# Optimization experiments

Hardware: AMD Instinct MI355X
Metric: run time of the kernel (lower is better)

The kernel has to match this reference:

```python
import jax, jax.numpy as jnp
import numpy as np

B, N, D, H = 4, 2048, 512, 8
DH = D // H
EPS = 1e-6


def setup_inputs() -> dict:
    key = jax.random.key(0)
    ks = jax.random.split(key, 12)
    s = 1.0 / np.sqrt(D)
    return {
        "x": jax.random.normal(ks[0], (B, N, D), jnp.float32),
        "attn_bias": jax.random.normal(ks[1], (B, 1, N, N), jnp.float32),
        "Wq": jax.random.normal(ks[2], (D, D), jnp.float32) * s,
        "bq": jnp.zeros((D,), jnp.float32),
        "Wk": jax.random.normal(ks[3], (D, D), jnp.float32) * s,
        "bk": jnp.zeros((D,), jnp.float32),
        "Wv": jax.random.normal(ks[4], (D, D), jnp.float32) * s,
        "bv": jnp.zeros((D,), jnp.float32),
        "Wo": jax.random.normal(ks[5], (D, D), jnp.float32) * s,
        "bo": jnp.zeros((D,), jnp.float32),
        "q_gamma": jnp.ones((DH,), jnp.float32),
        "q_beta": jnp.zeros((DH,), jnp.float32),
        "k_gamma": jnp.ones((DH,), jnp.float32),
        "k_beta": jnp.zeros((DH,), jnp.float32),
    }


def _layernorm(x, gamma, beta):
    mu = jnp.mean(x, axis=-1, keepdims=True)
    var = jnp.var(x, axis=-1, keepdims=True)
    return (x - mu) * jax.lax.rsqrt(var + EPS) * gamma + beta


def reference(x, attn_bias, Wq, bq, Wk, bk, Wv, bv, Wo, bo,
              q_gamma, q_beta, k_gamma, k_beta):
    b, n, d = x.shape
    # project and split heads: (B, H, N, DH)
    def heads(W, bias):
        return (x @ W.T + bias).reshape(b, n, H, DH).transpose(0, 2, 1, 3)
    q = heads(Wq, bq)
    k = heads(Wk, bk)
    v = heads(Wv, bv)
    q = _layernorm(q, q_gamma, q_beta)
    k = _layernorm(k, k_gamma, k_beta)
    scores = jnp.einsum('bhqd,bhkd->bhqk', q, k) / np.sqrt(DH)
    scores = scores + attn_bias  # (B,1,N,N) broadcasts over heads
    attn = jax.nn.softmax(scores, axis=-1)
    out = jnp.einsum('bhqk,bhkd->bhqd', attn, v)
    out = out.transpose(0, 2, 1, 3).reshape(b, n, d)
    return out @ Wo.T + bo
```

## Files before the change

kernel.cpp:

```cpp
#include <hip/hip_runtime.h>

typedef __attribute__((ext_vector_type(8))) short short8;
typedef __attribute__((ext_vector_type(4))) float f32x4;
typedef __attribute__((ext_vector_type(4))) int i32x4;
typedef __attribute__((ext_vector_type(4))) unsigned short u16x4;
typedef __attribute__((ext_vector_type(8))) unsigned short u16x8;
typedef __attribute__((ext_vector_type(2))) unsigned int u32x2;

#define B_  4
#define N_  2048
#define D_  512
#define H_  8
#define DH_ 64
#define M_  (B_ * N_)

__device__ __forceinline__ unsigned short f2bf(float f) {
    union { float f; unsigned u; } un; un.f = f;
    unsigned r = un.u + 0x7FFFu + ((un.u >> 16) & 1u);
    return (unsigned short)(r >> 16);
}
__device__ __forceinline__ float exp2fast(float x) {
#if __has_builtin(__builtin_amdgcn_exp2f)
    return __builtin_amdgcn_exp2f(x);
#else
    float r; asm("v_exp_f32 %0, %1" : "=v"(r) : "v"(x)); return r;
#endif
}
__device__ __forceinline__ unsigned cvtpk_bf16(float lo, float hi) {
    unsigned r;
    asm("v_cvt_pk_bf16_f32 %0, %1, %2" : "=v"(r) : "v"(lo), "v"(hi));
    return r;
}
__device__ __forceinline__ float max3f(float a, float b, float c) {
    return fmaxf(fmaxf(a, b), c);
}

typedef __attribute__((address_space(1))) const void gvoid;
typedef __attribute__((address_space(3))) void svoid;
__device__ __forceinline__ void load16_lds(const void* g, void* s) {
    __builtin_amdgcn_global_load_lds((gvoid*)g, (svoid*)s, 16, 0, 0);
}

__global__ __launch_bounds__(256) void cvt_all(
    const float* __restrict__ x,
    const float* __restrict__ W0, const float* __restrict__ W1,
    const float* __restrict__ W2, const float* __restrict__ W3,
    unsigned short* __restrict__ xb, unsigned short* __restrict__ Wb) {
    const int bx = blockIdx.x;
    const float* src;
    unsigned short* dst;
    int i;
    if (bx < 4096) {
        src = x; dst = xb;
        i = (bx * 256 + (int)threadIdx.x) * 4;
    } else {
        const int r = bx - 4096;
        const int sel = r >> 8;
        src = (sel == 0) ? W0 : (sel == 1) ? W1 : (sel == 2) ? W2 : W3;
        dst = Wb + (size_t)sel * D_ * D_;
        i = ((r & 255) * 256 + (int)threadIdx.x) * 4;
    }
    f32x4 v = *(const f32x4*)(src + i);
    u16x4 o;
    o[0] = f2bf(v[0]); o[1] = f2bf(v[1]); o[2] = f2bf(v[2]); o[3] = f2bf(v[3]);
    *(u16x4*)(dst + i) = o;
}

template <bool F32OUT, bool LNF>
__global__ __launch_bounds__(256, 2) void gemm_nt(
    const unsigned short* __restrict__ A,
    const unsigned short* __restrict__ W,
    const float* __restrict__ Bv0,
    const float* __restrict__ Bv1,
    const float* __restrict__ Bv2,
    const float* __restrict__ g0, const float* __restrict__ be0,
    const float* __restrict__ g1, const float* __restrict__ be1,
    unsigned short* __restrict__ outb,
    float* __restrict__ outf)
{
    const int mt = blockIdx.x;
    const int nt = blockIdx.y;
    const int sel = nt >> 2;
    const unsigned short* Wp = W + (size_t)sel * D_ * D_;
    const float* Bv = (sel == 0) ? Bv0 : (sel == 1) ? Bv1 : Bv2;
    const int n0 = (nt & 3) * 128;

    __shared__ __align__(16) unsigned short As[128 * 32];
    __shared__ __align__(16) unsigned short Bs[128 * 32];

    const int tid = threadIdx.x;
    const int w   = tid >> 6;
    const int l   = tid & 63;
    const int l15 = l & 15;
    const int qd  = l >> 4;
    const int wr  = w >> 1;
    const int wc  = w & 1;

    int srow[2], scol[2];
#pragma unroll
    for (int c = 0; c < 2; ++c) {
        const int g   = (w * 2 + c) * 64 + l;
        const int row = g >> 2;
        srow[c] = row;
        scol[c] = ((g & 3) ^ (row & 3)) * 8;
    }

    f32x4 acc[4][4];
#pragma unroll
    for (int i = 0; i < 4; ++i)
#pragma unroll
        for (int j = 0; j < 4; ++j)
            acc[i][j] = (f32x4){0.f, 0.f, 0.f, 0.f};

    const int swz = qd ^ (l15 & 3);

    for (int k0 = 0; k0 < D_; k0 += 32) {
        __syncthreads();
#pragma unroll
        for (int c = 0; c < 2; ++c) {
            load16_lds(A  + (size_t)(mt * 128 + srow[c]) * D_ + k0 + scol[c],
                       As + (w * 2 + c) * 512);
            load16_lds(Wp + (size_t)(n0 + srow[c]) * D_ + k0 + scol[c],
                       Bs + (w * 2 + c) * 512);
        }
        __syncthreads();

        short8 af[4], bfr[4];
#pragma unroll
        for (int rt = 0; rt < 4; ++rt)
            af[rt] = *(const short8*)&As[(wr * 64 + rt * 16 + l15) * 32 + swz * 8];
#pragma unroll
        for (int ct = 0; ct < 4; ++ct)
            bfr[ct] = *(const short8*)&Bs[(wc * 64 + ct * 16 + l15) * 32 + swz * 8];
#pragma unroll
        for (int rt = 0; rt < 4; ++rt)
#pragma unroll
            for (int ct = 0; ct < 4; ++ct)
                acc[rt][ct] = __builtin_amdgcn_mfma_f32_16x16x32_bf16(
                    af[rt], bfr[ct], acc[rt][ct], 0, 0, 0);
    }

    const float* gam = (sel == 0) ? g0 : g1;
    const float* bet = (sel == 0) ? be0 : be1;
    float gv[4], bv2[4];
    if (LNF) {
#pragma unroll
        for (int ct = 0; ct < 4; ++ct) { gv[ct] = gam[ct * 16 + l15]; bv2[ct] = bet[ct * 16 + l15]; }
    }

#pragma unroll
    for (int rt = 0; rt < 4; ++rt) {
        float v[4][4];
#pragma unroll
        for (int ct = 0; ct < 4; ++ct) {
            const float bias = Bv[n0 + wc * 64 + ct * 16 + l15];
#pragma unroll
            for (int r = 0; r < 4; ++r) v[ct][r] = acc[rt][ct][r] + bias;
        }
        if (LNF && sel < 2) {
#pragma unroll
            for (int r = 0; r < 4; ++r) {
                float s  = v[0][r] + v[1][r] + v[2][r] + v[3][r];
                float s2 = v[0][r]*v[0][r] + v[1][r]*v[1][r] + v[2][r]*v[2][r] + v[3][r]*v[3][r];
#pragma unroll
                for (int o = 1; o <= 8; o <<= 1) {
                    s  += __shfl_xor(s, o);
                    s2 += __shfl_xor(s2, o);
                }
                const float mu  = s * 0.015625f;
                const float var = s2 * 0.015625f - mu * mu;
                const float rs  = rsqrtf(var + 1e-6f);
#pragma unroll
                for (int ct = 0; ct < 4; ++ct)
                    v[ct][r] = (v[ct][r] - mu) * rs * gv[ct] + bv2[ct];
            }
        }
#pragma unroll
        for (int ct = 0; ct < 4; ++ct) {
            const int col  = n0 + wc * 64 + ct * 16 + l15;
            const int row0 = mt * 128 + wr * 64 + rt * 16 + qd * 4;
#pragma unroll
            for (int r = 0; r < 4; ++r) {
                const size_t oidx = (size_t)(row0 + r) * D_ + col;
                if (F32OUT) outf[oidx] = v[ct][r];
                else        outb[(size_t)sel * M_ * D_ + oidx] = f2bf(v[ct][r]);
            }
        }
    }
}

__global__ __launch_bounds__(256) void pack_kv(
    const unsigned short* __restrict__ K, const unsigned short* __restrict__ V,
    unsigned short* __restrict__ Kt, unsigned short* __restrict__ Vt2)
{
    const int nt = blockIdx.x, b = blockIdx.y;
    const int tid = threadIdx.x;
    __shared__ __align__(16) unsigned short Vl[64][520];

#pragma unroll
    for (int i = 0; i < 16; ++i) {
        const int c = i * 256 + tid;
        const int row = c >> 6, ch = c & 63;
        const size_t srow = ((size_t)(b * N_ + nt * 64 + row)) * D_ + ch * 8;
        i32x4 kd = *(const i32x4*)(K + srow);
        const int h = ch >> 3, dc = ch & 7;
        *(i32x4*)(Kt + ((((size_t)(b * 8 + h) * 32 + nt) * 64 + row) * 64) + dc * 8) = kd;
        i32x4 vd = *(const i32x4*)(V + srow);
        *(i32x4*)&Vl[row][ch * 8] = vd;
    }
    __syncthreads();
#pragma unroll
    for (int i = 0; i < 16; ++i) {
        const int c = i * 256 + tid;
        const int h = c >> 9, r = c & 511;
        const int dh = r >> 3, kc = r & 7;
        u16x4 o0, o1;
#pragma unroll
        for (int j = 0; j < 4; ++j) o0[j] = Vl[kc * 8 + j][h * 64 + dh];
#pragma unroll
        for (int j = 0; j < 4; ++j) o1[j] = Vl[kc * 8 + 4 + j][h * 64 + dh];
        const int t = kc >> 1;
        const int col0 = (t & 2) * 16 + (kc & 1) * 16 + (t & 1) * 4;
        const size_t rowbase = ((((size_t)(b * 8 + h) * 32 + nt) * 64 + dh) * 64);
        *(u16x4*)(Vt2 + rowbase + col0)     = o0;
        *(u16x4*)(Vt2 + rowbase + col0 + 8) = o1;
    }
}

__global__ __launch_bounds__(512, 4) void attn12(
    const unsigned short* __restrict__ Qm,
    const unsigned short* __restrict__ Kt,
    const unsigned short* __restrict__ Vt2,
    const float* __restrict__ Bias,
    unsigned short* __restrict__ AO)
{
    const int qt = blockIdx.x;
    const int h  = blockIdx.y;
    const int b  = blockIdx.z;
    const int w  = threadIdx.x >> 6;
    const int l  = threadIdx.x & 63;
    const int l15 = l & 15;
    const int qd  = l >> 4;
    const int q0 = qt * 128 + w * 16;
    const float L2E = 1.4426950408889634f;

    __shared__ __align__(16) unsigned char smem[32768];

    const int c    = w * 64 + l;
    const int srow = c >> 3;
    const int sg   = (c & 7) ^ (srow & 7);
    const int soff = srow * 64 + sg * 8;
    const int sc16 = c * 16;

    short8 qf[2];
#pragma unroll
    for (int hf = 0; hf < 2; ++hf)
        qf[hf] = *(const short8*)(Qm +
            (size_t)(b * N_ + q0 + l15) * D_ + h * DH_ + hf * 32 + qd * 8);

    f32x4 Ot[4];
#pragma unroll
    for (int rt = 0; rt < 4; ++rt) Ot[rt] = (f32x4){0.f, 0.f, 0.f, 0.f};
    float m_i = -3.0e38f;
    f32x4 li4 = (f32x4){0.f, 0.f, 0.f, 0.f};

    const unsigned short* Ktile0 = Kt  + (((size_t)(b * 8 + h) * 32) * 64) * 64;
    const unsigned short* Vtile0 = Vt2 + (((size_t)(b * 8 + h) * 32) * 64) * 64;
    const float* biasQ = Bias + ((size_t)b * N_ + q0 + l15) * N_;

    load16_lds(Ktile0 + soff, smem + sc16);
    load16_lds(Vtile0 + soff, smem + 8192 + sc16);
    f32x4 brA[4], brB[4];
#pragma unroll
    for (int rt = 0; rt < 4; ++rt)
        brA[rt] = *(const f32x4*)(biasQ + rt * 16 + qd * 4);
    asm volatile("s_waitcnt vmcnt(0)" ::: "memory");

#define ATTN_ITER(KT, CUR, BRC, BRN) do {                                      \
    unsigned char* Kbc = smem + (CUR) * 16384;                                 \
    unsigned char* Vbc = Kbc + 8192;                                           \
    asm volatile("s_waitcnt vmcnt(4)" ::: "memory");                           \
    __builtin_amdgcn_s_barrier();                                              \
    __builtin_amdgcn_sched_barrier(0);                                         \
    if ((KT) < 31) {                                                           \
        const unsigned short* Kn = Ktile0 + (size_t)((KT) + 1) * 4096;         \
        const unsigned short* Vn = Vtile0 + (size_t)((KT) + 1) * 4096;         \
        unsigned char* KbN = smem + (((CUR) ^ 1)) * 16384;                     \
        load16_lds(Kn + soff, KbN + sc16);                                     \
        load16_lds(Vn + soff, KbN + 8192 + sc16);                              \
    }                                                                          \
    asm volatile("" ::: "memory");       \
    {                                                                          \
        const float* Bn = biasQ + (size_t)(((KT) < 31) ? (KT) + 1 : 31) * 64;  \
        _Pragma("unroll")                                                      \
        for (int rt = 0; rt < 4; ++rt)                                         \
            BRN[rt] = *(const f32x4*)(Bn + rt * 16 + qd * 4);                  \
    }                                                                          \
    short8 kf[4][2];                                                           \
    _Pragma("unroll")                                                          \
    for (int rt = 0; rt < 4; ++rt) {                                           \
        const int kv = rt * 16 + l15;                                          \
        _Pragma("unroll")                                                      \
        for (int hf = 0; hf < 2; ++hf) {                                       \
            const int cidx = (hf * 4 + qd) ^ (kv & 7);                         \
            kf[rt][hf] = *(const short8*)(Kbc + kv * 128 + cidx * 16);         \
        }                                                                      \
    }                                                                          \
    f32x4 St[4];                                                               \
    __builtin_amdgcn_s_setprio(1);                                             \
    _Pragma("unroll")                                                          \
    for (int rt = 0; rt < 4; ++rt) {                                           \
        f32x4 v = (f32x4){0.f, 0.f, 0.f, 0.f};                                 \
        v = __builtin_amdgcn_mfma_f32_16x16x32_bf16(kf[rt][0], qf[0], v, 0, 0, 0); \
        v = __builtin_amdgcn_mfma_f32_16x16x32_bf16(kf[rt][1], qf[1], v, 0, 0, 0); \
        St[rt] = v;                                                            \
    }                                                                          \
    __builtin_amdgcn_s_setprio(0);                                             \
    short8 vf[4][2];                                                           \
    _Pragma("unroll")                                                          \
    for (int rt = 0; rt < 4; ++rt) {                                           \
        const int dh = rt * 16 + l15;                                          \
        _Pragma("unroll")                                                      \
        for (int hf = 0; hf < 2; ++hf) {                                       \
            const int cidx = (hf * 4 + qd) ^ (dh & 7);                         \
            vf[rt][hf] = *(const short8*)(Vbc + dh * 128 + cidx * 16);         \
        }                                                                      \
    }                                                                          \
    unsigned wq[4][2];                                                         \
    {                                                                          \
        f32x4 sv[4];                                                           \
        _Pragma("unroll")                                                      \
        for (int rt = 0; rt < 4; ++rt)                                         \
            sv[rt] = St[rt] * 0.125f + BRC[rt];                                \
        float mx0 = max3f(sv[0][0], sv[0][1], sv[0][2]);                       \
        float mx1 = max3f(sv[0][3], sv[1][0], sv[1][1]);                       \
        float mx2 = max3f(sv[1][2], sv[1][3], sv[2][0]);                       \
        float mx3 = max3f(sv[2][1], sv[2][2], sv[2][3]);                       \
        mx0 = max3f(mx0, sv[3][0], sv[3][1]);                                  \
        mx1 = max3f(mx1, sv[3][2], sv[3][3]);                                  \
        float mx = fmaxf(max3f(mx0, mx1, mx2), mx3);                           \
        mx = fmaxf(mx, __shfl_xor(mx, 16));                                    \
        mx = fmaxf(mx, __shfl_xor(mx, 32));                                    \
        if (__any(mx > m_i + 8.0f)) {                                          \
            const float mnew  = fmaxf(m_i, mx);                                \
            const float alpha = exp2fast((m_i - mnew) * L2E);                  \
            m_i = mnew;                                                        \
            li4 *= alpha;                                                      \
            _Pragma("unroll")                                                  \
            for (int rt = 0; rt < 4; ++rt) Ot[rt] *= alpha;                    \
        }                                                                      \
        const float mL = m_i * L2E;                                            \
        f32x4 p[4];                                                            \
        _Pragma("unroll")                                                      \
        for (int rt = 0; rt < 4; ++rt) {                                       \
            f32x4 e = sv[rt] * L2E - mL;                                       \
            p[rt][0] = exp2fast(e[0]); p[rt][1] = exp2fast(e[1]);              \
            p[rt][2] = exp2fast(e[2]); p[rt][3] = exp2fast(e[3]);              \
        }                                                                      \
        li4 += (p[0] + p[1]) + (p[2] + p[3]);                                  \
        _Pragma("unroll")                                                      \
        for (int rt = 0; rt < 4; ++rt) {                                       \
            wq[rt][0] = cvtpk_bf16(p[rt][0], p[rt][1]);                        \
            wq[rt][1] = cvtpk_bf16(p[rt][2], p[rt][3]);                        \
        }                                                                      \
    }                                                                          \
                           \
    union { unsigned u[4]; short8 s; } pk0, pk1;                               \
    pk0.u[0] = wq[0][0]; pk0.u[1] = wq[0][1];                                  \
    pk0.u[2] = wq[1][0]; pk0.u[3] = wq[1][1];                                  \
    pk1.u[0] = wq[2][0]; pk1.u[1] = wq[2][1];                                  \
    pk1.u[2] = wq[3][0]; pk1.u[3] = wq[3][1];                                  \
    __builtin_amdgcn_s_setprio(1);                                             \
    _Pragma("unroll")                                                          \
    for (int rt = 0; rt < 4; ++rt) {                                           \
        Ot[rt] = __builtin_amdgcn_mfma_f32_16x16x32_bf16(vf[rt][0], pk0.s, Ot[rt], 0, 0, 0); \
        Ot[rt] = __builtin_amdgcn_mfma_f32_16x16x32_bf16(vf[rt][1], pk1.s, Ot[rt], 0, 0, 0); \
    }                                                                          \
    __builtin_amdgcn_s_setprio(0);                                             \
} while (0)

    for (int kt2 = 0; kt2 < 16; ++kt2) {
        ATTN_ITER(kt2 * 2,     0, brA, brB);
        ATTN_ITER(kt2 * 2 + 1, 1, brB, brA);
    }
#undef ATTN_ITER

    float l_i = (li4[0] + li4[1]) + (li4[2] + li4[3]);
    l_i += __shfl_xor(l_i, 16);
    l_i += __shfl_xor(l_i, 32);
    const float inv = 1.f / l_i;
    const int q = q0 + l15;
#pragma unroll
    for (int rt = 0; rt < 4; ++rt) {
        u16x4 ob;
#pragma unroll
        for (int r = 0; r < 4; ++r) ob[r] = f2bf(Ot[rt][r] * inv);
        *(u16x4*)(AO + (size_t)(b * N_ + q) * D_ + h * DH_ + rt * 16 + qd * 4) = ob;
    }
}

extern "C" void kernel_launch(void* const* d_in, const int* in_sizes, int n_in,
                              void* d_out, int out_size, void* d_ws, size_t ws_size,
                              hipStream_t stream) {
    const float* x  = (const float*)d_in[0];
    const float* ab = (const float*)d_in[1];
    const float* Wq = (const float*)d_in[2];
    const float* bq = (const float*)d_in[3];
    const float* Wk = (const float*)d_in[4];
    const float* bk = (const float*)d_in[5];
    const float* Wv = (const float*)d_in[6];
    const float* bv = (const float*)d_in[7];
    const float* Wo = (const float*)d_in[8];
    const float* bo = (const float*)d_in[9];
    const float* qg = (const float*)d_in[10];
    const float* qb = (const float*)d_in[11];
    const float* kg = (const float*)d_in[12];
    const float* kb = (const float*)d_in[13];

    unsigned short* xb  = (unsigned short*)d_ws;
    unsigned short* Wb  = xb  + (size_t)M_ * D_;
    unsigned short* Y   = Wb  + (size_t)4 * D_ * D_;
    unsigned short* Kt  = Y   + (size_t)3 * M_ * D_;
    unsigned short* Vt2 = Kt  + (size_t)M_ * D_;
    unsigned short* AO  = Vt2 + (size_t)M_ * D_;
    float* out = (float*)d_out;

    cvt_all<<<dim3(5120), dim3(256), 0, stream>>>(x, Wq, Wk, Wv, Wo, xb, Wb);

    gemm_nt<false, true><<<dim3(64, 12), dim3(256), 0, stream>>>(
        xb, Wb, bq, bk, bv, qg, qb, kg, kb, Y, nullptr);

    pack_kv<<<dim3(32, 4), dim3(256), 0, stream>>>(
        Y + (size_t)M_ * D_, Y + (size_t)2 * M_ * D_, Kt, Vt2);

    attn12<<<dim3(16, 8, 4), dim3(512), 0, stream>>>(
        Y, Kt, Vt2, ab, AO);

    gemm_nt<true, false><<<dim3(64, 4), dim3(256), 0, stream>>>(
        AO, Wb + (size_t)3 * D_ * D_, bo, bo, bo,
        nullptr, nullptr, nullptr, nullptr, nullptr, out);
}
```

Baseline: 257.1 us.

## Fuse K/V packing into projection GEMM epilogues, double-buffer GEMM, shrink attention blocks

The pack_kv kernel is removed. K is written straight into its tiled layout from the QK projection epilogue, and V is computed as a transposed GEMM (Wv times x) whose epilogue writes the permuted Vt2 layout directly. The GEMM now double-buffers its LDS tiles so global loads overlap MFMA work. The attention kernel moves from 512-thread blocks over 128 queries to 256-thread blocks over 64 queries, which doubles the grid. This drops one launch and one full K/V round trip through memory, at the cost of scattered 2-byte epilogue stores that may coalesce poorly.

```diff
diff --git a/kernel.cpp b/kernel.cpp
--- a/kernel.cpp
+++ b/kernel.cpp
@@ -4,7 +4,6 @@
 typedef __attribute__((ext_vector_type(4))) float f32x4;
 typedef __attribute__((ext_vector_type(4))) int i32x4;
 typedef __attribute__((ext_vector_type(4))) unsigned short u16x4;
-typedef __attribute__((ext_vector_type(8))) unsigned short u16x8;
 typedef __attribute__((ext_vector_type(2))) unsigned int u32x2;
 
 #define B_  4
@@ -66,27 +65,26 @@
     *(u16x4*)(dst + i) = o;
 }
 
-template <bool F32OUT, bool LNF>
-__global__ __launch_bounds__(256, 2) void gemm_nt(
-    const unsigned short* __restrict__ A,
-    const unsigned short* __restrict__ W,
-    const float* __restrict__ Bv0,
-    const float* __restrict__ Bv1,
-    const float* __restrict__ Bv2,
+template <int MODE>
+__global__ __launch_bounds__(256, 2) void gemm2(
+    const unsigned short* __restrict__ Ain,
+    const unsigned short* __restrict__ Bin,
+    const float* __restrict__ BvQ, const float* __restrict__ BvK,
     const float* __restrict__ g0, const float* __restrict__ be0,
     const float* __restrict__ g1, const float* __restrict__ be1,
-    unsigned short* __restrict__ outb,
+    unsigned short* __restrict__ o1p,
+    unsigned short* __restrict__ o2p,
     float* __restrict__ outf)
 {
     const int mt = blockIdx.x;
     const int nt = blockIdx.y;
-    const int sel = nt >> 2;
-    const unsigned short* Wp = W + (size_t)sel * D_ * D_;
-    const float* Bv = (sel == 0) ? Bv0 : (sel == 1) ? Bv1 : Bv2;
-    const int n0 = (nt & 3) * 128;
-
-    __shared__ __align__(16) unsigned short As[128 * 32];
-    __shared__ __align__(16) unsigned short Bs[128 * 32];
+    int sel = 0, n0;
+    const unsigned short *Ap, *Bp;
+    if (MODE == 0) { sel = nt >> 2; n0 = (nt & 3) * 128; Ap = Ain; Bp = Bin + (size_t)sel * D_ * D_; }
+    else           { n0 = nt * 128; Ap = Ain; Bp = Bin; }
+
+    __shared__ __align__(16) unsigned short As[2][128 * 32];
+    __shared__ __align__(16) unsigned short Bs[2][128 * 32];
 
     const int tid = threadIdx.x;
     const int w   = tid >> 6;
@@ -96,13 +94,15 @@
     const int wr  = w >> 1;
     const int wc  = w & 1;
 
-    int srow[2], scol[2];
+    const unsigned short* Asrc[2];
+    const unsigned short* Bsrc[2];
 #pragma unroll
     for (int c = 0; c < 2; ++c) {
         const int g   = (w * 2 + c) * 64 + l;
         const int row = g >> 2;
-        srow[c] = row;
-        scol[c] = ((g & 3) ^ (row & 3)) * 8;
+        const int sc  = ((g & 3) ^ (row & 3)) * 8;
+        Asrc[c] = Ap + (size_t)(mt * 128 + row) * D_ + sc;
+        Bsrc[c] = Bp + (size_t)(n0 + row) * D_ + sc;
     }
 
     f32x4 acc[4][4];
@@ -114,39 +114,91 @@
 
     const int swz = qd ^ (l15 & 3);
 
-    for (int k0 = 0; k0 < D_; k0 += 32) {
-        __syncthreads();
-#pragma unroll
-        for (int c = 0; c < 2; ++c) {
-            load16_lds(A  + (size_t)(mt * 128 + srow[c]) * D_ + k0 + scol[c],
-                       As + (w * 2 + c) * 512);
-            load16_lds(Wp + (size_t)(n0 + srow[c]) * D_ + k0 + scol[c],
-                       Bs + (w * 2 + c) * 512);
-        }
-        __syncthreads();
+#define GSTAGE(bb, kk) do {                                                    \
+    _Pragma("unroll")                                                          \
+    for (int c2 = 0; c2 < 2; ++c2) {                                           \
+        load16_lds(Asrc[c2] + (kk) * 32, &As[bb][(w * 2 + c2) * 512]);         \
+        load16_lds(Bsrc[c2] + (kk) * 32, &Bs[bb][(w * 2 + c2) * 512]);         \
+    }                                                                          \
+} while (0)
+
+    GSTAGE(0, 0);
+    asm volatile("s_waitcnt vmcnt(0)" ::: "memory");
+    __builtin_amdgcn_s_barrier();
+    __builtin_amdgcn_sched_barrier(0);
+
+    for (int k = 0; k < 16; ++k) {
+        const int bb = k & 1;
+        if (k < 15) GSTAGE(bb ^ 1, k + 1);
 
         short8 af[4], bfr[4];
 #pragma unroll
         for (int rt = 0; rt < 4; ++rt)
-            af[rt] = *(const short8*)&As[(wr * 64 + rt * 16 + l15) * 32 + swz * 8];
+            af[rt] = *(const short8*)&As[bb][(wr * 64 + rt * 16 + l15) * 32 + swz * 8];
 #pragma unroll
         for (int ct = 0; ct < 4; ++ct)
-            bfr[ct] = *(const short8*)&Bs[(wc * 64 + ct * 16 + l15) * 32 + swz * 8];
+            bfr[ct] = *(const short8*)&Bs[bb][(wc * 64 + ct * 16 + l15) * 32 + swz * 8];
 #pragma unroll
         for (int rt = 0; rt < 4; ++rt)
 #pragma unroll
             for (int ct = 0; ct < 4; ++ct)
                 acc[rt][ct] = __builtin_amdgcn_mfma_f32_16x16x32_bf16(
                     af[rt], bfr[ct], acc[rt][ct], 0, 0, 0);
-    }
-
+
+        asm volatile("s_waitcnt vmcnt(0)" ::: "memory");
+        __builtin_amdgcn_s_barrier();
+        __builtin_amdgcn_sched_barrier(0);
+    }
+#undef GSTAGE
+
+    if (MODE == 1) {
+#pragma unroll
+        for (int rt = 0; rt < 4; ++rt) {
+            const int row0 = mt * 128 + wr * 64 + rt * 16 + qd * 4;
+            float bvr[4];
+#pragma unroll
+            for (int r = 0; r < 4; ++r) bvr[r] = BvQ[row0 + r];
+#pragma unroll
+            for (int ct = 0; ct < 4; ++ct) {
+                const int col = n0 + wc * 64 + ct * 16 + l15;
+                const int b2 = col >> 11, n = col & 2047;
+                const int nt64 = n >> 6, kv = n & 63;
+                const int colp = ((kv >> 5) & 1) * 32 + ((kv >> 3) & 1) * 16 +
+                                 ((kv >> 4) & 1) * 4  + ((kv >> 2) & 1) * 8 + (kv & 3);
+#pragma unroll
+                for (int r = 0; r < 4; ++r) {
+                    const int ch = row0 + r;
+                    const int h = ch >> 6, dh = ch & 63;
+                    o1p[(((size_t)(b2 * 8 + h) * 32 + nt64) * 64 + dh) * 64 + colp] =
+                        f2bf(acc[rt][ct][r] + bvr[r]);
+                }
+            }
+        }
+        return;
+    }
+
+    if (MODE == 2) {
+#pragma unroll
+        for (int rt = 0; rt < 4; ++rt) {
+#pragma unroll
+            for (int ct = 0; ct < 4; ++ct) {
+                const int col = n0 + wc * 64 + ct * 16 + l15;
+                const float bias = BvQ[col];
+                const int row0 = mt * 128 + wr * 64 + rt * 16 + qd * 4;
+#pragma unroll
+                for (int r = 0; r < 4; ++r)
+                    outf[(size_t)(row0 + r) * D_ + col] = acc[rt][ct][r] + bias;
+            }
+        }
+        return;
+    }
+
+    const float* Bv  = (sel == 0) ? BvQ : BvK;
     const float* gam = (sel == 0) ? g0 : g1;
     const float* bet = (sel == 0) ? be0 : be1;
     float gv[4], bv2[4];
-    if (LNF) {
-#pragma unroll
-        for (int ct = 0; ct < 4; ++ct) { gv[ct] = gam[ct * 16 + l15]; bv2[ct] = bet[ct * 16 + l15]; }
-    }
+#pragma unroll
+    for (int ct = 0; ct < 4; ++ct) { gv[ct] = gam[ct * 16 + l15]; bv2[ct] = bet[ct * 16 + l15]; }
 
 #pragma unroll
     for (int rt = 0; rt < 4; ++rt) {
@@ -157,77 +209,46 @@
 #pragma unroll
             for (int r = 0; r < 4; ++r) v[ct][r] = acc[rt][ct][r] + bias;
         }
-        if (LNF && sel < 2) {
-#pragma unroll
-            for (int r = 0; r < 4; ++r) {
-                float s  = v[0][r] + v[1][r] + v[2][r] + v[3][r];
-                float s2 = v[0][r]*v[0][r] + v[1][r]*v[1][r] + v[2][r]*v[2][r] + v[3][r]*v[3][r];
-#pragma unroll
-                for (int o = 1; o <= 8; o <<= 1) {
-                    s  += __shfl_xor(s, o);
-                    s2 += __shfl_xor(s2, o);
-                }
-                const float mu  = s * 0.015625f;
-                const float var = s2 * 0.015625f - mu * mu;
-                const float rs  = rsqrtf(var + 1e-6f);
-#pragma unroll
-                for (int ct = 0; ct < 4; ++ct)
-                    v[ct][r] = (v[ct][r] - mu) * rs * gv[ct] + bv2[ct];
+#pragma unroll
+        for (int r = 0; r < 4; ++r) {
+            float s  = v[0][r] + v[1][r] + v[2][r] + v[3][r];
+            float s2 = v[0][r]*v[0][r] + v[1][r]*v[1][r] + v[2][r]*v[2][r] + v[3][r]*v[3][r];
+#pragma unroll
+            for (int o = 1; o <= 8; o <<= 1) {
+                s  += __shfl_xor(s, o);
+                s2 += __shfl_xor(s2, o);
             }
+            const float mu  = s * 0.015625f;
+            const float var = s2 * 0.015625f - mu * mu;
+            const float rs  = rsqrtf(var + 1e-6f);
+#pragma unroll
+            for (int ct = 0; ct < 4; ++ct)
+                v[ct][r] = (v[ct][r] - mu) * rs * gv[ct] + bv2[ct];
         }
 #pragma unroll
         for (int ct = 0; ct < 4; ++ct) {
             const int col  = n0 + wc * 64 + ct * 16 + l15;
             const int row0 = mt * 128 + wr * 64 + rt * 16 + qd * 4;
-#pragma unroll
-            for (int r = 0; r < 4; ++r) {
-                const size_t oidx = (size_t)(row0 + r) * D_ + col;
-                if (F32OUT) outf[oidx] = v[ct][r];
-                else        outb[(size_t)sel * M_ * D_ + oidx] = f2bf(v[ct][r]);
+            if (sel == 0) {
+#pragma unroll
+                for (int r = 0; r < 4; ++r)
+                    o1p[(size_t)(row0 + r) * D_ + col] = f2bf(v[ct][r]);
+            } else {
+                const int h = col >> 6, dh = col & 63;
+#pragma unroll
+                for (int r = 0; r < 4; ++r) {
+                    const int row = row0 + r;
+                    const int b2 = row >> 11, n = row & 2047;
+                    const int nt64 = n >> 6, kvr = n & 63;
+                    o2p[(((size_t)(b2 * 8 + h) * 32 + nt64) * 64 + kvr) * 64 + dh] =
+                        f2bf(v[ct][r]);
+                }
             }
         }
     }
 }
 
-__global__ __launch_bounds__(256) void pack_kv(
-    const unsigned short* __restrict__ K, const unsigned short* __restrict__ V,
-    unsigned short* __restrict__ Kt, unsigned short* __restrict__ Vt2)
-{
-    const int nt = blockIdx.x, b = blockIdx.y;
-    const int tid = threadIdx.x;
-    __shared__ __align__(16) unsigned short Vl[64][520];
-
-#pragma unroll
-    for (int i = 0; i < 16; ++i) {
-        const int c = i * 256 + tid;
-        const int row = c >> 6, ch = c & 63;
-        const size_t srow = ((size_t)(b * N_ + nt * 64 + row)) * D_ + ch * 8;
-        i32x4 kd = *(const i32x4*)(K + srow);
-        const int h = ch >> 3, dc = ch & 7;
-        *(i32x4*)(Kt + ((((size_t)(b * 8 + h) * 32 + nt) * 64 + row) * 64) + dc * 8) = kd;
-        i32x4 vd = *(const i32x4*)(V + srow);
-        *(i32x4*)&Vl[row][ch * 8] = vd;
-    }
-    __syncthreads();
-#pragma unroll
-    for (int i = 0; i < 16; ++i) {
-        const int c = i * 256 + tid;
-        const int h = c >> 9, r = c & 511;
-        const int dh = r >> 3, kc = r & 7;
-        u16x4 o0, o1;
-#pragma unroll
-        for (int j = 0; j < 4; ++j) o0[j] = Vl[kc * 8 + j][h * 64 + dh];
-#pragma unroll
-        for (int j = 0; j < 4; ++j) o1[j] = Vl[kc * 8 + 4 + j][h * 64 + dh];
-        const int t = kc >> 1;
-        const int col0 = (t & 2) * 16 + (kc & 1) * 16 + (t & 1) * 4;
-        const size_t rowbase = ((((size_t)(b * 8 + h) * 32 + nt) * 64 + dh) * 64);
-        *(u16x4*)(Vt2 + rowbase + col0)     = o0;
-        *(u16x4*)(Vt2 + rowbase + col0 + 8) = o1;
-    }
-}
-
-__global__ __launch_bounds__(512, 4) void attn12(
+__global__ __launch_bounds__(256, 4) void attn13(
     const unsigned short* __restrict__ Qm,
     const unsigned short* __restrict__ Kt,
     const unsigned short* __restrict__ Vt2,
@@ -241,16 +262,20 @@
     const int l  = threadIdx.x & 63;
     const int l15 = l & 15;
     const int qd  = l >> 4;
-    const int q0 = qt * 128 + w * 16;
+    const int q0 = qt * 64 + w * 16;
     const float L2E = 1.4426950408889634f;
 
     __shared__ __align__(16) unsigned char smem[32768];
 
-    const int c    = w * 64 + l;
-    const int srow = c >> 3;
-    const int sg   = (c & 7) ^ (srow & 7);
-    const int soff = srow * 64 + sg * 8;
-    const int sc16 = c * 16;
+    int soff[2], sc16[2];
+#pragma unroll
+    for (int i = 0; i < 2; ++i) {
+        const int c = (w * 2 + i) * 64 + l;
+        const int srow = c >> 3;
+        const int sg   = (c & 7) ^ (srow & 7);
+        soff[i] = srow * 64 + sg * 8;
+        sc16[i] = c * 16;
+    }
 
     short8 qf[2];
 #pragma unroll
@@ -268,8 +293,11 @@
     const unsigned short* Vtile0 = Vt2 + (((size_t)(b * 8 + h) * 32) * 64) * 64;
     const float* biasQ = Bias + ((size_t)b * N_ + q0 + l15) * N_;
 
-    load16_lds(Ktile0 + soff, smem + sc16);
-    load16_lds(Vtile0 + soff, smem + 8192 + sc16);
+#pragma unroll
+    for (int i = 0; i < 2; ++i) {
+        load16_lds(Ktile0 + soff[i], smem + sc16[i]);
+        load16_lds(Vtile0 + soff[i], smem + 8192 + sc16[i]);
+    }
     f32x4 brA[4], brB[4];
 #pragma unroll
     for (int rt = 0; rt < 4; ++rt)
@@ -286,8 +314,11 @@
         const unsigned short* Kn = Ktile0 + (size_t)((KT) + 1) * 4096;         \
         const unsigned short* Vn = Vtile0 + (size_t)((KT) + 1) * 4096;         \
         unsigned char* KbN = smem + (((CUR) ^ 1)) * 16384;                     \
-        load16_lds(Kn + soff, KbN + sc16);                                     \
-        load16_lds(Vn + soff, KbN + 8192 + sc16);                              \
+        _Pragma("unroll")                                                      \
+        for (int i = 0; i < 2; ++i) {                                          \
+            load16_lds(Kn + soff[i], KbN + sc16[i]);                           \
+            load16_lds(Vn + soff[i], KbN + 8192 + sc16[i]);                    \
+        }                                                                      \
     }                                                                          \
     asm volatile("" ::: "memory");       \
     {                                                                          \
@@ -364,7 +395,6 @@
             wq[rt][1] = cvtpk_bf16(p[rt][2], p[rt][3]);                        \
         }                                                                      \
     }                                                                          \
-                           \
     union { unsigned u[4]; short8 s; } pk0, pk1;                               \
     pk0.u[0] = wq[0][0]; pk0.u[1] = wq[0][1];                                  \
     pk0.u[2] = wq[1][0]; pk0.u[3] = wq[1][1];                                  \
@@ -419,24 +449,25 @@
 
     unsigned short* xb  = (unsigned short*)d_ws;
     unsigned short* Wb  = xb  + (size_t)M_ * D_;
-    unsigned short* Y   = Wb  + (size_t)4 * D_ * D_;
-    unsigned short* Kt  = Y   + (size_t)3 * M_ * D_;
+    unsigned short* Yq  = Wb  + (size_t)4 * D_ * D_;
+    unsigned short* Kt  = Yq  + (size_t)M_ * D_;
     unsigned short* Vt2 = Kt  + (size_t)M_ * D_;
     unsigned short* AO  = Vt2 + (size_t)M_ * D_;
     float* out = (float*)d_out;
 
     cvt_all<<<dim3(5120), dim3(256), 0, stream>>>(x, Wq, Wk, Wv, Wo, xb, Wb);
 
-    gemm_nt<false, true><<<dim3(64, 12), dim3(256), 0, stream>>>(
-        xb, Wb, bq, bk, bv, qg, qb, kg, kb, Y, nullptr);
-
-    pack_kv<<<dim3(32, 4), dim3(256), 0, stream>>>(
-        Y + (size_t)M_ * D_, Y + (size_t)2 * M_ * D_, Kt, Vt2);
-
-    attn12<<<dim3(16, 8, 4), dim3(512), 0, stream>>>(
-        Y, Kt, Vt2, ab, AO);
-
-    gemm_nt<true, false><<<dim3(64, 4), dim3(256), 0, stream>>>(
-        AO, Wb + (size_t)3 * D_ * D_, bo, bo, bo,
-        nullptr, nullptr, nullptr, nullptr, nullptr, out);
-}
+    gemm2<0><<<dim3(64, 8), dim3(256), 0, stream>>>(
+        xb, Wb, bq, bk, qg, qb, kg, kb, Yq, Kt, nullptr);
+
+    gemm2<1><<<dim3(4, 64), dim3(256), 0, stream>>>(
+        Wb + (size_t)2 * D_ * D_, xb, bv, nullptr,
+        nullptr, nullptr, nullptr, nullptr, Vt2, nullptr, nullptr);
+
+    attn13<<<dim3(32, 8, 4), dim3(256), 0, stream>>>(
+        Yq, Kt, Vt2, ab, AO);
+
+    gemm2<2><<<dim3(64, 4), dim3(256), 0, stream>>>(
+        AO, Wb + (size_t)3 * D_ * D_, bo, nullptr,
+        nullptr, nullptr, nullptr, nullptr, nullptr, nullptr, out);
+}
```

After: 275.0 us. +6.9%, slower.
